# Performance work log

Measured on AMD Instinct MI355X. Metric: run time of the kernel, lower is better.

The kernel has to match this reference:

```python
import jax, jax.numpy as jnp
import numpy as np

B, Q, KV, D, H = 2, 2048, 2048, 1024, 16
HD = D // H  # head dim = 64


def setup_inputs() -> dict:
    key = jax.random.key(0)
    ks = jax.random.split(key, 16)
    s = 1.0 / np.sqrt(D)
    return {
        "q": jax.random.normal(ks[0], (B, Q, D), jnp.float32),
        "k": jax.random.normal(ks[1], (B, KV, D), jnp.float32),
        "v": jax.random.normal(ks[2], (B, KV, D), jnp.float32),
        "past_k": jax.random.normal(ks[3], (B, KV, D), jnp.float32),
        "past_v": jax.random.normal(ks[4], (B, KV, D), jnp.float32),
        "mask": jax.random.randint(ks[5], (B, Q, KV + KV), 0, 2).astype(bool),
        "Wq": jax.random.uniform(ks[6], (D, D), jnp.float32, -s, s),
        "bq": jax.random.uniform(ks[7], (D,), jnp.float32, -s, s),
        "Wk": jax.random.uniform(ks[8], (D, D), jnp.float32, -s, s),
        "bk": jax.random.uniform(ks[9], (D,), jnp.float32, -s, s),
        "Wv": jax.random.uniform(ks[10], (D, D), jnp.float32, -s, s),
        "bv": jax.random.uniform(ks[11], (D,), jnp.float32, -s, s),
        "Wl": jax.random.uniform(ks[12], (D, D), jnp.float32, -s, s),
        "bl": jax.random.uniform(ks[13], (D,), jnp.float32, -s, s),
    }


def _split_heads(x):
    # (B, S, D) -> (B, H, S, HD)
    b, s, _ = x.shape
    return x.reshape(b, s, H, HD).transpose(0, 2, 1, 3)


def reference(q, k, v, past_k, past_v, mask, Wq, bq, Wk, bk, Wv, bv, Wl, bl):
    qp = q @ Wq.T + bq
    kp = k @ Wk.T + bk
    vp = v @ Wv.T + bv
    k_cat = jnp.concatenate([past_k, kp], axis=-2)  # (B, P+KV, D)
    v_cat = jnp.concatenate([past_v, vp], axis=-2)
    qh = _split_heads(qp)        # (B, H, Q, HD)
    kh = _split_heads(k_cat)     # (B, H, P+KV, HD)
    vh = _split_heads(v_cat)
    scores = jnp.einsum("bhqd,bhkd->bhqk", qh, kh) / np.sqrt(HD)
    scores = scores + mask[:, None].astype(scores.dtype) * (-10000.0)
    attn = jax.nn.softmax(scores, axis=-1)
    out = jnp.einsum("bhqk,bhkd->bhqd", attn, vh)  # (B, H, Q, HD)
    out = out.transpose(0, 2, 1, 3).reshape(q.shape[0], q.shape[1], D)
    x = out @ Wl.T + bl
    return (x, k_cat, v_cat)
```

## Files before the change

### kernel.cpp

```cpp
#include <hip/hip_runtime.h>

#define QLEN 2048
#define KVTOT 4096
#define DMODEL 1024
#define MASKC2 -14427.0f
#define SENT2  -28854.0f

typedef __attribute__((ext_vector_type(8))) short bf16x8;
typedef __attribute__((ext_vector_type(4))) float f32x4;
typedef unsigned short u16;
typedef unsigned int u32;
typedef unsigned long long u64;

__device__ __forceinline__ u16 f2b(float f) {
  union { float f; unsigned u; } v; v.f = f;
  unsigned r = v.u + 0x7FFFu + ((v.u >> 16) & 1u);
  return (u16)(r >> 16);
}

__device__ __forceinline__ u32 cvt_pk_bf16(float lo, float hi) {
  u32 r;
  asm("v_cvt_pk_bf16_f32 %0, %1, %2" : "=v"(r) : "v"(lo), "v"(hi));
  return r;
}

__device__ __forceinline__ float exp2v(float x) {
  float r;
  asm("v_exp_f32 %0, %1" : "=v"(r) : "v"(x));
  return r;
}

__device__ __forceinline__ float max3f(float a, float b, float c) {
  float r;
  asm("v_max3_f32 %0, %1, %2, %3" : "=v"(r) : "v"(a), "v"(b), "v"(c));
  return r;
}

__device__ __forceinline__ void gll16(const u16* g, u16* l) {
  __builtin_amdgcn_global_load_lds(
      (const __attribute__((address_space(1))) u32*)g,
      (__attribute__((address_space(3))) u32*)l, 16, 0, 0);
}

__global__ __launch_bounds__(256) void copy_past(
    const float* __restrict__ pk, const float* __restrict__ pv,
    float* __restrict__ kcat, float* __restrict__ vcat,
    u16* __restrict__ kh) {
  int i = blockIdx.x * 256 + threadIdx.x;
  int b = i >> 19;
  int r = i & 524287;
  size_t src = (size_t)i * 4;
  size_t dst = ((size_t)b * 1048576 + r) * 4;
  float4 kk = *(const float4*)&pk[src];
  float4 vv = *(const float4*)&pv[src];
  *(float4*)&kcat[dst] = kk;
  *(float4*)&vcat[dst] = vv;
  int s = r >> 8;
  int c4 = (r & 255) * 4;
  int h = c4 >> 6, d = c4 & 63;
  uint2 w = make_uint2(cvt_pk_bf16(kk.x, kk.y), cvt_pk_bf16(kk.z, kk.w));
  *(uint2*)&kh[((size_t)(b * 16 + h) * KVTOT + s) * 64 + d] = w;
}

__global__ __launch_bounds__(256) void maskpack(
    const int* __restrict__ mask, u64* __restrict__ bits) {
  int w = blockIdx.x * 4 + (threadIdx.x >> 6);
  int lane = threadIdx.x & 63;
  int mv = mask[(size_t)w * 64 + lane];
  u64 b = __ballot(mv != 0);
  if (lane == 0) bits[w] = b;
}

__global__ __launch_bounds__(256) void w2b(
    const float* __restrict__ w0, const float* __restrict__ w1,
    const float* __restrict__ w2, const float* __restrict__ w3,
    u16* __restrict__ dst) {
  const float* src = blockIdx.y == 0 ? w0 : blockIdx.y == 1 ? w1
                   : blockIdx.y == 2 ? w2 : w3;
  size_t i = ((size_t)blockIdx.x * 256 + threadIdx.x) * 8;
  float4 a = *(const float4*)&src[i];
  float4 b = *(const float4*)&src[i + 4];
  uint4 o = {cvt_pk_bf16(a.x, a.y), cvt_pk_bf16(a.z, a.w),
             cvt_pk_bf16(b.x, b.y), cvt_pk_bf16(b.z, b.w)};
  *(uint4*)&dst[(size_t)blockIdx.y * 1048576 + i] = o;
}

__global__ __launch_bounds__(256) void gemm_qkv(
    const float* __restrict__ qA, const float* __restrict__ kA,
    const float* __restrict__ vA, const u16* __restrict__ Wb,
    const float* __restrict__ bq, const float* __restrict__ bk,
    const float* __restrict__ bv,
    u16* __restrict__ qh, float* __restrict__ kcat, u16* __restrict__ kh,
    float* __restrict__ vcat) {
  const int K = 1024, N = 1024;
  __shared__ u16 As[128][32];
  __shared__ u16 Bs[128][32];
  const int z = blockIdx.z;
  const float* A = (z == 0) ? qA : (z == 1) ? kA : vA;
  const u16* W = Wb + (size_t)z * 1048576;
  const float* bias = (z == 0) ? bq : (z == 1) ? bk : bv;
  const int t = threadIdx.x;
  const int m0 = blockIdx.y * 128, n0 = blockIdx.x * 128;
  const int lane = t & 63, wid = t >> 6;
  const int wr = (wid >> 1) * 64, wc = (wid & 1) * 64;
  const int lr = lane & 15, lg = lane >> 4;
  const int ko = lg * 8;

  f32x4 acc[4][4];
  #pragma unroll
  for (int m = 0; m < 4; ++m)
    #pragma unroll
    for (int n = 0; n < 4; ++n)
      acc[m][n] = (f32x4){0.f, 0.f, 0.f, 0.f};

  for (int k0 = 0; k0 < K; k0 += 32) {
    float4 a0[2], a1[2];
    #pragma unroll
    for (int j = 0; j < 2; ++j) {
      int idx = t + j * 256;
      int r = idx >> 2, c8 = (idx & 3) * 8;
      const float* ap = A + (size_t)(m0 + r) * K + k0 + c8;
      a0[j] = *(const float4*)ap;
      a1[j] = *(const float4*)(ap + 4);
    }
    __syncthreads();
    #pragma unroll
    for (int j = 0; j < 2; ++j) {
      int idx = t + j * 256;
      int r = idx >> 2, c8 = (idx & 3) * 8;
      gll16(W + (size_t)(n0 + r) * K + k0 + c8,
            &Bs[0][0] + (size_t)(j * 256 + (t & ~63)) * 8);
      uint4 o = {cvt_pk_bf16(a0[j].x, a0[j].y), cvt_pk_bf16(a0[j].z, a0[j].w),
                 cvt_pk_bf16(a1[j].x, a1[j].y), cvt_pk_bf16(a1[j].z, a1[j].w)};
      *(uint4*)&As[r][c8] = o;
    }
    __syncthreads();
    bf16x8 av[4], bv4[4];
    #pragma unroll
    for (int m = 0; m < 4; ++m)
      av[m] = *(const bf16x8*)&As[wr + m * 16 + lr][ko];
    #pragma unroll
    for (int n = 0; n < 4; ++n)
      bv4[n] = *(const bf16x8*)&Bs[wc + n * 16 + lr][ko];
    #pragma unroll
    for (int m = 0; m < 4; ++m)
      #pragma unroll
      for (int n = 0; n < 4; ++n)
        acc[m][n] = __builtin_amdgcn_mfma_f32_16x16x32_bf16(av[m], bv4[n], acc[m][n], 0, 0, 0);
  }

  const int rq = lg * 4;
  #pragma unroll
  for (int m = 0; m < 4; ++m) {
    #pragma unroll
    for (int r = 0; r < 4; ++r) {
      int row = m0 + wr + m * 16 + rq + r;
      int bb = row >> 11, s = row & 2047;
      #pragma unroll
      for (int n = 0; n < 4; ++n) {
        int col = n0 + wc + n * 16 + lr;
        float val = acc[m][n][r] + bias[col];
        int hh = col >> 6, d = col & 63;
        if (z == 0) {
          qh[((size_t)(bb * 16 + hh) * QLEN + s) * 64 + d] = f2b(val * 0.18033688f);
        } else if (z == 1) {
          kcat[(size_t)(bb * 4096 + 2048 + s) * 1024 + col] = val;
          kh[((size_t)(bb * 16 + hh) * KVTOT + 2048 + s) * 64 + d] = f2b(val);
        } else {
          vcat[(size_t)(bb * 4096 + 2048 + s) * 1024 + col] = val;
        }
      }
    }
  }
}

__global__ __launch_bounds__(256) void gemm_out(
    const u16* __restrict__ A, const u16* __restrict__ W,
    const float* __restrict__ bias, float* __restrict__ C) {
  const int K = 1024, N = 1024;
  __shared__ u16 As[128][32];
  __shared__ u16 Bs[128][32];
  const int t = threadIdx.x;
  const int m0 = blockIdx.y * 128, n0 = blockIdx.x * 128;
  const int lane = t & 63, wid = t >> 6;
  const int wr = (wid >> 1) * 64, wc = (wid & 1) * 64;
  const int lr = lane & 15, lg = lane >> 4;
  const int ko = lg * 8;

  f32x4 acc[4][4];
  #pragma unroll
  for (int m = 0; m < 4; ++m)
    #pragma unroll
    for (int n = 0; n < 4; ++n)
      acc[m][n] = (f32x4){0.f, 0.f, 0.f, 0.f};

  for (int k0 = 0; k0 < K; k0 += 32) {
    __syncthreads();
    #pragma unroll
    for (int j = 0; j < 2; ++j) {
      int idx = t + j * 256;
      int r = idx >> 2, c8 = (idx & 3) * 8;
      size_t ldsoff = (size_t)(j * 256 + (t & ~63)) * 8;
      gll16(A + (size_t)(m0 + r) * K + k0 + c8, &As[0][0] + ldsoff);
      gll16(W + (size_t)(n0 + r) * K + k0 + c8, &Bs[0][0] + ldsoff);
    }
    __syncthreads();
    bf16x8 av[4], bv4[4];
    #pragma unroll
    for (int m = 0; m < 4; ++m)
      av[m] = *(const bf16x8*)&As[wr + m * 16 + lr][ko];
    #pragma unroll
    for (int n = 0; n < 4; ++n)
      bv4[n] = *(const bf16x8*)&Bs[wc + n * 16 + lr][ko];
    #pragma unroll
    for (int m = 0; m < 4; ++m)
      #pragma unroll
      for (int n = 0; n < 4; ++n)
        acc[m][n] = __builtin_amdgcn_mfma_f32_16x16x32_bf16(av[m], bv4[n], acc[m][n], 0, 0, 0);
  }

  const int rq = lg * 4;
  #pragma unroll
  for (int m = 0; m < 4; ++m) {
    #pragma unroll
    for (int r = 0; r < 4; ++r) {
      int row = m0 + wr + m * 16 + rq + r;
      float* cp = C + (size_t)row * N;
      #pragma unroll
      for (int n = 0; n < 4; ++n) {
        int col = n0 + wc + n * 16 + lr;
        cp[col] = acc[m][n][r] + bias[col];
      }
    }
  }
}

__global__ __launch_bounds__(256) void repack_vt(
    const float* __restrict__ src, u16* __restrict__ dst) {
  __shared__ u16 T[64][72];
  const int t = threadIdx.x;
  const int kv0 = blockIdx.x * 64;
  const int bh = blockIdx.y;
  const int b = bh >> 4, h = bh & 15;
  #pragma unroll
  for (int it = 0; it < 4; ++it) {
    int idx = t + it * 256;
    int r = idx >> 4;
    int c4 = (idx & 15) * 4;
    float4 v = *(const float4*)(src + (size_t)(b * KVTOT + kv0 + r) * DMODEL + h * 64 + c4);
    *(uint2*)&T[r][c4] = make_uint2(cvt_pk_bf16(v.x, v.y), cvt_pk_bf16(v.z, v.w));
  }
  __syncthreads();
  #pragma unroll
  for (int it = 0; it < 2; ++it) {
    int idx = t + it * 256;
    int d = idx & 63;
    int kc8 = (idx >> 6) * 8;
    bf16x8 o;
    #pragma unroll
    for (int j = 0; j < 8; ++j) o[j] = (short)T[kc8 + j][d];
    *(bf16x8*)(dst + (size_t)((b * 16 + h) * 64 + d) * KVTOT + kv0 + kc8) = o;
  }
}

__global__ __launch_bounds__(256, 2) void attn_mfma(
    const u16* __restrict__ qh, const u16* __restrict__ kh,
    const u16* __restrict__ vt, const u64* __restrict__ mbits,
    u16* __restrict__ out) {
  __shared__ float mO[4][64][68];
  __shared__ float mM[4][64];
  __shared__ float mL[4][64];
  __shared__ u16 Pl[4][16][72];
  const int t = threadIdx.x;
  const int wid = t >> 6, lane = t & 63;
  const int lr = lane & 15, lg = lane >> 4;
  const int fid = blockIdx.x;
  const int virt = (fid & 7) * 128 + (fid >> 3);
  const int bh = virt >> 5, qt = virt & 31;
  const int b = bh >> 4, h = bh & 15;
  const int q0 = qt * 64;

  bf16x8 ones;
  #pragma unroll
  for (int j = 0; j < 8; ++j) ones[j] = (short)0x3F80;

  bf16x8 qf[4][2];
  #pragma unroll
  for (int i = 0; i < 4; ++i) {
    const u16* qp = qh + ((size_t)bh * QLEN + q0 + i * 16 + lr) * 64 + lg * 8;
    qf[i][0] = *(const bf16x8*)qp;
    qf[i][1] = *(const bf16x8*)(qp + 32);
  }

  const u16* kbase = kh + (size_t)bh * KVTOT * 64 + (size_t)wid * 1024 * 64;
  const u16* vbase = vt + (size_t)bh * 64 * KVTOT + wid * 1024;
  const u64* mbase = mbits + ((size_t)b * QLEN + q0 + lr) * 64 + wid * 16;

  float mprev[4] = {SENT2, SENT2, SENT2, SENT2};
  f32x4 oacc[4][4];
  f32x4 oaccL[4];
  #pragma unroll
  for (int i = 0; i < 4; ++i) {
    oaccL[i] = (f32x4){0.f, 0.f, 0.f, 0.f};
    #pragma unroll
    for (int dt = 0; dt < 4; ++dt) oacc[i][dt] = (f32x4){0.f, 0.f, 0.f, 0.f};
  }

  bf16x8 kf[4][2];
  #pragma unroll
  for (int tile = 0; tile < 4; ++tile) {
    const u16* kp = kbase + (size_t)(tile * 16 + lr) * 64 + lg * 8;
    kf[tile][0] = *(const bf16x8*)kp;
    kf[tile][1] = *(const bf16x8*)(kp + 32);
  }

  for (int it = 0; it < 16; ++it) {
    bf16x8 vf[4][2];
    const u16* vp = vbase + it * 64;
    #pragma unroll
    for (int dt = 0; dt < 4; ++dt) {
      const u16* vq = vp + (size_t)(dt * 16 + lr) * KVTOT + lg * 8;
      vf[dt][0] = *(const bf16x8*)vq;
      vf[dt][1] = *(const bf16x8*)(vq + 32);
    }

    #pragma unroll
    for (int i = 0; i < 4; ++i) {
      u64 mb = mbase[(size_t)i * 1024 + it];
      u64 mq = mb >> (lg * 4);
      const float negm = -mprev[i], negmm = MASKC2 - mprev[i];
      f32x4 sacc[4];
      #pragma unroll
      for (int tile = 0; tile < 4; ++tile) {
        unsigned nib = (unsigned)((mq >> (tile * 16)) & 0xFull);
        #pragma unroll
        for (int r = 0; r < 4; ++r)
          sacc[tile][r] = (nib & (1u << r)) ? negmm : negm;
      }
      __builtin_amdgcn_s_setprio(1);
      #pragma unroll
      for (int tile = 0; tile < 4; ++tile) {
        sacc[tile] = __builtin_amdgcn_mfma_f32_16x16x32_bf16(kf[tile][0], qf[i][0], sacc[tile], 0, 0, 0);
        sacc[tile] = __builtin_amdgcn_mfma_f32_16x16x32_bf16(kf[tile][1], qf[i][1], sacc[tile], 0, 0, 0);
      }
      __builtin_amdgcn_s_setprio(0);

      if (i == 3 && it + 1 < 16) {
        const u16* kp = kbase + (size_t)(it + 1) * 4096;
        #pragma unroll
        for (int tile = 0; tile < 4; ++tile) {
          const u16* kq = kp + (size_t)(tile * 16 + lr) * 64 + lg * 8;
          kf[tile][0] = *(const bf16x8*)kq;
          kf[tile][1] = *(const bf16x8*)(kq + 32);
        }
      }

      float t1 = max3f(sacc[0][0], sacc[0][1], sacc[0][2]);
      float t2 = max3f(sacc[0][3], sacc[1][0], sacc[1][1]);
      float t3 = max3f(sacc[1][2], sacc[1][3], sacc[2][0]);
      float t4 = max3f(sacc[2][1], sacc[2][2], sacc[2][3]);
      float t5 = max3f(sacc[3][0], sacc[3][1], sacc[3][2]);
      float rmax = fmaxf(sacc[3][3], t1);
      rmax = max3f(rmax, t2, t3);
      rmax = max3f(rmax, t4, t5);
      rmax = fmaxf(rmax, __shfl_xor(rmax, 16));
      rmax = fmaxf(rmax, __shfl_xor(rmax, 32));

      if (!__all(rmax <= 11.0f)) {
        float shift = fmaxf(rmax, 0.f);
        float corr = exp2v(-shift);
        float cr[4];
        #pragma unroll
        for (int r = 0; r < 4; ++r) cr[r] = __shfl(corr, lg * 4 + r);
        #pragma unroll
        for (int dt = 0; dt < 4; ++dt)
          #pragma unroll
          for (int r = 0; r < 4; ++r) oacc[i][dt][r] *= cr[r];
        #pragma unroll
        for (int r = 0; r < 4; ++r) oaccL[i][r] *= cr[r];
        mprev[i] += shift;
        #pragma unroll
        for (int tile = 0; tile < 4; ++tile)
          #pragma unroll
          for (int r = 0; r < 4; ++r) sacc[tile][r] -= shift;
      }

      #pragma unroll
      for (int tile = 0; tile < 4; ++tile) {
        float p0 = exp2v(sacc[tile][0]);
        float p1 = exp2v(sacc[tile][1]);
        float p2 = exp2v(sacc[tile][2]);
        float p3 = exp2v(sacc[tile][3]);
        *(uint2*)&Pl[wid][lr][tile * 16 + lg * 4] =
            make_uint2(cvt_pk_bf16(p0, p1), cvt_pk_bf16(p2, p3));
      }
      bf16x8 pa0 = *(const bf16x8*)&Pl[wid][lr][lg * 8];
      bf16x8 pa1 = *(const bf16x8*)&Pl[wid][lr][32 + lg * 8];

      __builtin_amdgcn_s_setprio(1);
      #pragma unroll
      for (int dt = 0; dt < 4; ++dt) {
        oacc[i][dt] = __builtin_amdgcn_mfma_f32_16x16x32_bf16(pa0, vf[dt][0], oacc[i][dt], 0, 0, 0);
        oacc[i][dt] = __builtin_amdgcn_mfma_f32_16x16x32_bf16(pa1, vf[dt][1], oacc[i][dt], 0, 0, 0);
      }
      oaccL[i] = __builtin_amdgcn_mfma_f32_16x16x32_bf16(pa0, ones, oaccL[i], 0, 0, 0);
      oaccL[i] = __builtin_amdgcn_mfma_f32_16x16x32_bf16(pa1, ones, oaccL[i], 0, 0, 0);
      __builtin_amdgcn_s_setprio(0);
    }
  }

  #pragma unroll
  for (int i = 0; i < 4; ++i)
    #pragma unroll
    for (int dt = 0; dt < 4; ++dt)
      #pragma unroll
      for (int r = 0; r < 4; ++r)
        mO[wid][i * 16 + lg * 4 + r][dt * 16 + lr] = oacc[i][dt][r];
  if (lr == 0) {
    #pragma unroll
    for (int i = 0; i < 4; ++i)
      #pragma unroll
      for (int r = 0; r < 4; ++r)
        mL[wid][i * 16 + lg * 4 + r] = oaccL[i][r];
  }
  if (lg == 0) {
    #pragma unroll
    for (int i = 0; i < 4; ++i) mM[wid][i * 16 + lr] = mprev[i];
  }
  __syncthreads();

  const int q = wid * 16 + lr;
  float m0 = mM[0][q], m1 = mM[1][q], m2 = mM[2][q], m3 = mM[3][q];
  float mm = fmaxf(max3f(m0, m1, m2), m3);
  float w0 = exp2v(m0 - mm), w1 = exp2v(m1 - mm);
  float w2 = exp2v(m2 - mm), w3 = exp2v(m3 - mm);
  float l = mL[0][q] * w0 + mL[1][q] * w1 + mL[2][q] * w2 + mL[3][q] * w3;
  float inv = 1.f / l;
  float o[16];
  #pragma unroll
  for (int c = 0; c < 4; ++c) {
    f32x4 a0 = *(const f32x4*)&mO[0][q][lg * 16 + c * 4];
    f32x4 a1 = *(const f32x4*)&mO[1][q][lg * 16 + c * 4];
    f32x4 a2 = *(const f32x4*)&mO[2][q][lg * 16 + c * 4];
    f32x4 a3 = *(const f32x4*)&mO[3][q][lg * 16 + c * 4];
    #pragma unroll
    for (int j = 0; j < 4; ++j)
      o[c * 4 + j] = (a0[j] * w0 + a1[j] * w1 + a2[j] * w2 + a3[j] * w3) * inv;
  }
  u16* op = out + ((size_t)b * QLEN + q0 + q) * DMODEL + h * 64 + lg * 16;
  uint4 wA = {cvt_pk_bf16(o[0], o[1]), cvt_pk_bf16(o[2], o[3]),
              cvt_pk_bf16(o[4], o[5]), cvt_pk_bf16(o[6], o[7])};
  uint4 wB = {cvt_pk_bf16(o[8], o[9]), cvt_pk_bf16(o[10], o[11]),
              cvt_pk_bf16(o[12], o[13]), cvt_pk_bf16(o[14], o[15])};
  *(uint4*)op = wA;
  *(uint4*)(op + 8) = wB;
}

extern "C" void kernel_launch(void* const* d_in, const int* in_sizes, int n_in,
                              void* d_out, int out_size, void* d_ws, size_t ws_size,
                              hipStream_t stream) {
  const float* q      = (const float*)d_in[0];
  const float* k      = (const float*)d_in[1];
  const float* v      = (const float*)d_in[2];
  const float* past_k = (const float*)d_in[3];
  const float* past_v = (const float*)d_in[4];
  const int*   mask   = (const int*)d_in[5];
  const float* Wq     = (const float*)d_in[6];
  const float* bq     = (const float*)d_in[7];
  const float* Wk     = (const float*)d_in[8];
  const float* bk     = (const float*)d_in[9];
  const float* Wv     = (const float*)d_in[10];
  const float* bv     = (const float*)d_in[11];
  const float* Wl     = (const float*)d_in[12];
  const float* bl     = (const float*)d_in[13];

  float* xout = (float*)d_out;
  float* kcat = xout + 4194304;
  float* vcat = xout + 12582912;

  u16* wsb = (u16*)d_ws;
  u16* attno = wsb;
  u16* qh = wsb + 4194304;
  u16* kh = wsb + 8388608;
  u16* vt = wsb + 16777216;
  u16* Wb = wsb + 25165824;
  u64* mbits = (u64*)(wsb + 29360128);

  copy_past<<<4096, 256, 0, stream>>>(past_k, past_v, kcat, vcat, kh);
  maskpack<<<65536, 256, 0, stream>>>(mask, mbits);
  w2b<<<dim3(512, 4), 256, 0, stream>>>(Wq, Wk, Wv, Wl, Wb);

  gemm_qkv<<<dim3(8, 32, 3), 256, 0, stream>>>(
      q, k, v, Wb, bq, bk, bv, qh, kcat, kh, vcat);

  repack_vt<<<dim3(64, 32), 256, 0, stream>>>(vcat, vt);

  attn_mfma<<<1024, 256, 0, stream>>>(qh, kh, vt, mbits, attno);

  gemm_out<<<dim3(8, 32), 256, 0, stream>>>(attno, Wb + 3145728, bl, xout);
}
```

Before: 332.1 us.

## Shrink attention LDS via bf16 merge buffer aliased with P tile, raise occupancy

The fp32 cross-wave merge buffer and the separate P staging tile are replaced by one shared bf16 buffer used for both, which cuts LDS per block roughly in half. Launch bounds go from 2 to 4 blocks per CU to exploit the freed space, and the mask words for all four row groups are loaded up front each iteration. Rounding the partial outputs to bf16 before the merge adds precision loss, and the higher occupancy target limits registers per thread and may cause spills given the large accumulator set.

```diff
diff --git a/kernel.cpp b/kernel.cpp
--- a/kernel.cpp
+++ b/kernel.cpp
@@ -16,6 +16,10 @@
   union { float f; unsigned u; } v; v.f = f;
   unsigned r = v.u + 0x7FFFu + ((v.u >> 16) & 1u);
   return (u16)(r >> 16);
+}
+
+__device__ __forceinline__ float b2f(u16 x) {
+  union { u32 u; float f; } v; v.u = (u32)x << 16; return v.f;
 }
 
 __device__ __forceinline__ u32 cvt_pk_bf16(float lo, float hi) {
@@ -263,14 +267,13 @@
   }
 }
 
-__global__ __launch_bounds__(256, 2) void attn_mfma(
+__global__ __launch_bounds__(256, 4) void attn_mfma(
     const u16* __restrict__ qh, const u16* __restrict__ kh,
     const u16* __restrict__ vt, const u64* __restrict__ mbits,
     u16* __restrict__ out) {
-  __shared__ float mO[4][64][68];
+  __shared__ __align__(16) u16 shm[4 * 64 * 72];
   __shared__ float mM[4][64];
   __shared__ float mL[4][64];
-  __shared__ u16 Pl[4][16][72];
   const int t = threadIdx.x;
   const int wid = t >> 6, lane = t & 63;
   const int lr = lane & 15, lg = lane >> 4;
@@ -280,6 +283,8 @@
   const int b = bh >> 4, h = bh & 15;
   const int q0 = qt * 64;
 
+  u16* Plw = shm + wid * 1152;
+
   bf16x8 ones;
   #pragma unroll
   for (int j = 0; j < 8; ++j) ones[j] = (short)0x3F80;
@@ -315,6 +320,10 @@
   }
 
   for (int it = 0; it < 16; ++it) {
+    u64 mbv[4];
+    #pragma unroll
+    for (int i = 0; i < 4; ++i) mbv[i] = mbase[(size_t)i * 1024 + it];
+
     bf16x8 vf[4][2];
     const u16* vp = vbase + it * 64;
     #pragma unroll
@@ -326,8 +335,7 @@
 
     #pragma unroll
     for (int i = 0; i < 4; ++i) {
-      u64 mb = mbase[(size_t)i * 1024 + it];
-      u64 mq = mb >> (lg * 4);
+      u64 mq = mbv[i] >> (lg * 4);
       const float negm = -mprev[i], negmm = MASKC2 - mprev[i];
       f32x4 sacc[4];
       #pragma unroll
@@ -391,11 +399,11 @@
         float p1 = exp2v(sacc[tile][1]);
         float p2 = exp2v(sacc[tile][2]);
         float p3 = exp2v(sacc[tile][3]);
-        *(uint2*)&Pl[wid][lr][tile * 16 + lg * 4] =
+        *(uint2*)&Plw[lr * 72 + tile * 16 + lg * 4] =
             make_uint2(cvt_pk_bf16(p0, p1), cvt_pk_bf16(p2, p3));
       }
-      bf16x8 pa0 = *(const bf16x8*)&Pl[wid][lr][lg * 8];
-      bf16x8 pa1 = *(const bf16x8*)&Pl[wid][lr][32 + lg * 8];
+      bf16x8 pa0 = *(const bf16x8*)&Plw[lr * 72 + lg * 8];
+      bf16x8 pa1 = *(const bf16x8*)&Plw[lr * 72 + 32 + lg * 8];
 
       __builtin_amdgcn_s_setprio(1);
       #pragma unroll
@@ -409,13 +417,15 @@
     }
   }
 
+  __syncthreads();
+  u16* mo = shm + wid * 4608;
   #pragma unroll
   for (int i = 0; i < 4; ++i)
     #pragma unroll
     for (int dt = 0; dt < 4; ++dt)
       #pragma unroll
       for (int r = 0; r < 4; ++r)
-        mO[wid][i * 16 + lg * 4 + r][dt * 16 + lr] = oacc[i][dt][r];
+        mo[(i * 16 + lg * 4 + r) * 72 + dt * 16 + lr] = f2b(oacc[i][dt][r]);
   if (lr == 0) {
     #pragma unroll
     for (int i = 0; i < 4; ++i)
@@ -436,16 +446,20 @@
   float w2 = exp2v(m2 - mm), w3 = exp2v(m3 - mm);
   float l = mL[0][q] * w0 + mL[1][q] * w1 + mL[2][q] * w2 + mL[3][q] * w3;
   float inv = 1.f / l;
+  float wgt[4] = {w0 * inv, w1 * inv, w2 * inv, w3 * inv};
   float o[16];
   #pragma unroll
-  for (int c = 0; c < 4; ++c) {
-    f32x4 a0 = *(const f32x4*)&mO[0][q][lg * 16 + c * 4];
-    f32x4 a1 = *(const f32x4*)&mO[1][q][lg * 16 + c * 4];
-    f32x4 a2 = *(const f32x4*)&mO[2][q][lg * 16 + c * 4];
-    f32x4 a3 = *(const f32x4*)&mO[3][q][lg * 16 + c * 4];
-    #pragma unroll
-    for (int j = 0; j < 4; ++j)
-      o[c * 4 + j] = (a0[j] * w0 + a1[j] * w1 + a2[j] * w2 + a3[j] * w3) * inv;
+  for (int j = 0; j < 16; ++j) o[j] = 0.f;
+  #pragma unroll
+  for (int w = 0; w < 4; ++w) {
+    const u16* src = shm + w * 4608 + q * 72 + lg * 16;
+    bf16x8 a0 = *(const bf16x8*)src;
+    bf16x8 a1 = *(const bf16x8*)(src + 8);
+    #pragma unroll
+    for (int j = 0; j < 8; ++j) {
+      o[j]     += b2f((u16)a0[j]) * wgt[w];
+      o[8 + j] += b2f((u16)a1[j]) * wgt[w];
+    }
   }
   u16* op = out + ((size_t)b * QLEN + q0 + q) * DMODEL + h * 64 + lg * 16;
   uint4 wA = {cvt_pk_bf16(o[0], o[1]), cvt_pk_bf16(o[2], o[3]),
```

Measured after the change: 982.6 us. 196% more time.
